# Kernel tuning notes

Measured on AMD Instinct MI355X. Metric: run time of the kernel, lower is better.

The kernel has to match this reference:

```python
import jax, jax.numpy as jnp
import numpy as np

V, D, F, B, E = 50257, 1024, 2048, 64, 512  # vocab, embed/rnn dim, fc hidden, batch, entities


def setup_inputs() -> dict:
    key = jax.random.key(0)
    ks = jax.random.split(key, 12)
    s = 0.05
    return {
        "entity_hiddens": jax.random.normal(ks[0], (B, E, D), jnp.float32),
        "question": jax.random.randint(ks[1], (B,), 0, V),
        "keys_mask": jax.random.randint(ks[2], (B, E), 0, 2).astype(bool),
        "emb": jax.random.normal(ks[3], (V, D), jnp.float32) * s,
        "W1": jax.random.normal(ks[4], (D, F), jnp.float32) * s,
        "b1": jnp.zeros((F,), jnp.float32),
        "W2": jax.random.normal(ks[5], (F, D), jnp.float32) * s,
        "b2": jnp.zeros((D,), jnp.float32),
        "A": jax.random.normal(ks[6], (D, D), jnp.float32) * s,  # entity_attn_matrix
        "H": jax.random.normal(ks[7], (D, D), jnp.float32) * s,
        "Ws": jax.random.normal(ks[8], (D, V), jnp.float32) * s,
        "bs": jnp.zeros((V,), jnp.float32),
    }


def reference(entity_hiddens, question, keys_mask, emb, W1, b1, W2, b2, A, H, Ws, bs):
    # embed question token and project: [B, D]
    eq0 = emb[question]
    q = jax.nn.relu(eq0 @ W1 + b1) @ W2 + b2
    # attention_entities actual returned math:
    # reduce_sum(expand_dims(q@A,1) * boolean_mask(entities, mask), axis=1)
    # == (q @ A) * sum over all masked entities (a single [D] vector)
    qA = q @ A  # [B, D]
    m = keys_mask.astype(entity_hiddens.dtype)
    ent_sum = jnp.sum(entity_hiddens * m[..., None], axis=(0, 1))  # [D]
    u = qA * ent_sum  # [B, D]
    logits = (q + u @ H) @ Ws + bs  # [B, V]
    return jax.nn.softmax(logits, axis=-1)
```

## Files before the change

kernel.cpp:

```cpp
#include <hip/hip_runtime.h>
#include <stdint.h>

#define V_ 50257
#define D_ 1024
#define F_ 2048
#define B_ 64
#define E_ 512
#define ROWS_ (B_*E_)

typedef __attribute__((ext_vector_type(8))) short bf16x8;
typedef __attribute__((ext_vector_type(4))) float f32x4;

__device__ __forceinline__ unsigned rne1(float a) {
  unsigned u = __float_as_uint(a);
  return (u + 0x7FFFu + ((u >> 16) & 1u)) >> 16;
}

__device__ __forceinline__ float waveMax(float v) {
#pragma unroll
  for (int o = 32; o > 0; o >>= 1) v = fmaxf(v, __shfl_xor(v, o, 64));
  return v;
}
__device__ __forceinline__ float waveSum(float v) {
#pragma unroll
  for (int o = 32; o > 0; o >>= 1) v += __shfl_xor(v, o, 64);
  return v;
}


__device__ __forceinline__ void ent_partial_body(int bid, const float* __restrict__ eh,
                                                 const void* __restrict__ mask,
                                                 float* __restrict__ part) {
  __shared__ int s_mode;
  const int tid = threadIdx.x;
  const uint32_t* mu = (const uint32_t*)mask;
  int f = 0;
  for (int i = tid; i < (ROWS_ / 4); i += 256) {
    uint32_t u = mu[i];
    if (u == 0x3F800000u) f |= 2;
    else if (u & 0xFFFFFF00u) f |= 1;
  }
  if (tid == 0) s_mode = 0;
  __syncthreads();
  if (f) atomicOr(&s_mode, f);
  __syncthreads();
  const int sm = s_mode;
  const int mode = (sm & 1) ? 1 : ((sm & 2) ? 2 : 0);

  float4 acc = make_float4(0.f, 0.f, 0.f, 0.f);
  const float4* eh4 = (const float4*)eh;
  for (int row = bid; row < ROWS_; row += 512) {
    bool on;
    if (mode == 1)      on = ((const unsigned char*)mask)[row] != 0;
    else if (mode == 2) on = ((const float*)mask)[row] != 0.f;
    else                on = ((const int*)mask)[row] != 0;
    if (on) {
      float4 v = eh4[(size_t)row * (D_ / 4) + tid];
      acc.x += v.x; acc.y += v.y; acc.z += v.z; acc.w += v.w;
    }
  }
  ((float4*)part)[(size_t)bid * (D_ / 4) + tid] = acc;
}

__device__ __forceinline__ void ent_reduce_body(int bid, const float* __restrict__ part,
                                                float* __restrict__ entsum) {
  int d = bid * 256 + threadIdx.x;
  float s0 = 0.f, s1 = 0.f, s2 = 0.f, s3 = 0.f;
  for (int i = 0; i < 512; i += 4) {
    s0 += part[(size_t)(i    ) * D_ + d];
    s1 += part[(size_t)(i + 1) * D_ + d];
    s2 += part[(size_t)(i + 2) * D_ + d];
    s3 += part[(size_t)(i + 3) * D_ + d];
  }
  entsum[d] = (s0 + s1) + (s2 + s3);
}

__device__ __forceinline__ void gemm64_body(int bx, int by, const float* __restrict__ X,
                                            const int* __restrict__ gatherIdx,
                                            const float* __restrict__ emb,
                                            const float* __restrict__ W,
                                            int K, int N, int KB, float* __restrict__ part) {
  const int l  = threadIdx.x & 63;
  const int rg = __builtin_amdgcn_readfirstlane((int)(threadIdx.x >> 6));
  const int c  = bx * 64 + l;
  const int k0 = by * KB;
  const int m0 = rg * 16;

  const float* Xp = gatherIdx ? emb : X;
  int rb[16];
#pragma unroll
  for (int r = 0; r < 16; ++r) {
    int m = m0 + r;
    rb[r] = gatherIdx ? gatherIdx[m] * K : m * K;
  }

  float acc[16];
#pragma unroll
  for (int r = 0; r < 16; ++r) acc[r] = 0.f;

  for (int k = k0; k < k0 + KB; k += 8) {
    float wv[8];
#pragma unroll
    for (int j = 0; j < 8; ++j) wv[j] = W[(size_t)(k + j) * N + c];
#pragma unroll
    for (int r = 0; r < 16; ++r) {
      float4 x0 = *(const float4*)&Xp[rb[r] + k];
      float4 x1 = *(const float4*)&Xp[rb[r] + k + 4];
      acc[r] = fmaf(x0.x, wv[0], acc[r]);
      acc[r] = fmaf(x0.y, wv[1], acc[r]);
      acc[r] = fmaf(x0.z, wv[2], acc[r]);
      acc[r] = fmaf(x0.w, wv[3], acc[r]);
      acc[r] = fmaf(x1.x, wv[4], acc[r]);
      acc[r] = fmaf(x1.y, wv[5], acc[r]);
      acc[r] = fmaf(x1.z, wv[6], acc[r]);
      acc[r] = fmaf(x1.w, wv[7], acc[r]);
    }
  }
  size_t base = (size_t)by * ((size_t)64 * N);
#pragma unroll
  for (int r = 0; r < 16; ++r) part[base + (size_t)(m0 + r) * N + c] = acc[r];
}

__device__ __forceinline__ void reduce_ep_body(int bid, const float* __restrict__ part,
                                               int nsplit, int MN, int N,
                                               const float* __restrict__ vecB,
                                               const float* __restrict__ addend,
                                               int mode, float* __restrict__ dst,
                                               unsigned short* __restrict__ dhi,
                                               unsigned short* __restrict__ dlo) {
  int idx = bid * 256 + threadIdx.x;
  if (idx >= MN) return;
  float s = 0.f;
  for (int i = 0; i < nsplit; ++i) s += part[(size_t)i * MN + idx];
  int c = idx & (N - 1);
  if (mode == 1)      { s += vecB[c]; s = s > 0.f ? s : 0.f; dst[idx] = s; }
  else if (mode == 2) { s += vecB[c]; dst[idx] = s; }
  else if (mode == 3) { s *= vecB[c]; dst[idx] = s; }
  else {
    s += addend[idx];
    unsigned hi = rne1(s);
    float hif = __uint_as_float(hi << 16);
    dhi[idx] = (unsigned short)hi;
    dlo[idx] = (unsigned short)rne1(s - hif);
  }
}

__global__ void k_p1(const float* __restrict__ eh, const void* __restrict__ mask,
                     float* __restrict__ entpart, const int* __restrict__ ques,
                     const float* __restrict__ emb, const float* __restrict__ W1,
                     float* __restrict__ gpart) {
  int bid = blockIdx.x;
  if (bid < 512) ent_partial_body(bid, eh, mask, entpart);
  else {
    int b2 = bid - 512;
    gemm64_body(b2 & 31, b2 >> 5, nullptr, ques, emb, W1, 1024, 2048, 64, gpart);
  }
}

__global__ void k_p2(const float* __restrict__ entpart, float* __restrict__ entsum,
                     const float* __restrict__ gpart, const float* __restrict__ b1,
                     float* __restrict__ hbuf) {
  int bid = blockIdx.x;
  if (bid < 4) ent_reduce_body(bid, entpart, entsum);
  else reduce_ep_body(bid - 4, gpart, 16, 64 * 2048, 2048, b1, nullptr, 1, hbuf, nullptr, nullptr);
}

__global__ void k_gemm64(const float* __restrict__ X, const float* __restrict__ W,
                         int K, int N, int KB, float* __restrict__ part) {
  gemm64_body(blockIdx.x, blockIdx.y, X, nullptr, nullptr, W, K, N, KB, part);
}

__global__ void k_reduce_ep(const float* __restrict__ part, int nsplit, int MN, int N,
                            const float* __restrict__ vecB, const float* __restrict__ addend,
                            int mode, float* __restrict__ dst,
                            unsigned short* __restrict__ dhi, unsigned short* __restrict__ dlo) {
  reduce_ep_body(blockIdx.x, part, nsplit, MN, N, vecB, addend, mode, dst, dhi, dlo);
}

__global__ __launch_bounds__(512, 1) void k_gemm_big(const unsigned short* __restrict__ zhi,
                                                     const unsigned short* __restrict__ zlo,
                                                     const float* __restrict__ Ws,
                                                     float* __restrict__ part2) {
  __shared__ float lds[2][32 * 514];
  const int t   = threadIdx.x;
  const int l   = t & 63;
  const int w   = t >> 6;
  const int col = l & 15;
  const int g   = l >> 4;
  const int c0  = blockIdx.x * 512;
  const int kbase = blockIdx.y * 512;

  int scol[8];
#pragma unroll
  for (int j = 0; j < 8; ++j) {
    int s = c0 + j * 64 + l;
    scol[j] = s < V_ ? s : V_ - 1;
  }

  unsigned aoff[4];
#pragma unroll
  for (int m = 0; m < 4; ++m) aoff[m] = (unsigned)((m * 16 + col) * D_ + g * 8);

  f32x4 acc[4][4];
#pragma unroll
  for (int n = 0; n < 4; ++n)
#pragma unroll
    for (int m = 0; m < 4; ++m) acc[n][m] = (f32x4){0.f, 0.f, 0.f, 0.f};

#pragma unroll
  for (int i = 0; i < 4; ++i) {
    const int r = w * 4 + i;
#pragma unroll
    for (int j = 0; j < 8; ++j) {
      __builtin_amdgcn_global_load_lds(
          (const __attribute__((address_space(1))) void*)(Ws + (size_t)(kbase + r) * V_ + scol[j]),
          (__attribute__((address_space(3))) void*)&lds[0][r * 514 + j * 64],
          4, 0, 0);
    }
  }
  __syncthreads();

  for (int it = 0; it < 16; ++it) {
    const int buf = it & 1;
    const int k0  = kbase + it * 32;

    bf16x8 ah[4], al[4];
#pragma unroll
    for (int m = 0; m < 4; ++m) {
      ah[m] = *(const bf16x8*)(zhi + aoff[m] + k0);
      al[m] = *(const bf16x8*)(zlo + aoff[m] + k0);
    }

    if (it + 1 < 16) {
      const float* wb = Ws + (size_t)(k0 + 32) * V_;
#pragma unroll
      for (int i = 0; i < 4; ++i) {
        const int r = w * 4 + i;
#pragma unroll
        for (int j = 0; j < 8; ++j) {
          __builtin_amdgcn_global_load_lds(
              (const __attribute__((address_space(1))) void*)(wb + (size_t)r * V_ + scol[j]),
              (__attribute__((address_space(3))) void*)&lds[buf ^ 1][r * 514 + j * 64],
              4, 0, 0);
        }
      }
    }

#pragma unroll
    for (int n = 0; n < 4; ++n) {
      float f[8];
#pragma unroll
      for (int j = 0; j < 8; ++j)
        f[j] = lds[buf][(g * 8 + j) * 514 + w * 64 + n * 16 + col];

      union { bf16x8 v; unsigned u[4]; } bh, bl;
#pragma unroll
      for (int j = 0; j < 4; ++j) {
        unsigned h0 = rne1(f[2 * j]);
        unsigned h1 = rne1(f[2 * j + 1]);
        float h0f = __uint_as_float(h0 << 16);
        float h1f = __uint_as_float(h1 << 16);
        bh.u[j] = h0 | (h1 << 16);
        bl.u[j] = rne1(f[2 * j] - h0f) | (rne1(f[2 * j + 1] - h1f) << 16);
      }
#pragma unroll
      for (int m = 0; m < 4; ++m) acc[n][m] = __builtin_amdgcn_mfma_f32_16x16x32_bf16(ah[m], bh.v, acc[n][m], 0, 0, 0);
#pragma unroll
      for (int m = 0; m < 4; ++m) acc[n][m] = __builtin_amdgcn_mfma_f32_16x16x32_bf16(ah[m], bl.v, acc[n][m], 0, 0, 0);
#pragma unroll
      for (int m = 0; m < 4; ++m) acc[n][m] = __builtin_amdgcn_mfma_f32_16x16x32_bf16(al[m], bh.v, acc[n][m], 0, 0, 0);
    }

    __syncthreads();
  }

  float* pout = part2 + (size_t)blockIdx.y * ((size_t)64 * V_);
#pragma unroll
  for (int n = 0; n < 4; ++n) {
    const int c = c0 + w * 64 + n * 16 + col;
    if (c < V_) {
#pragma unroll
      for (int m = 0; m < 4; ++m)
#pragma unroll
        for (int i = 0; i < 4; ++i)
          pout[(size_t)(m * 16 + g * 4 + i) * V_ + c] = acc[n][m][i];
    }
  }
}

#define SM_CHUNK 12565

__global__ void k_redbias(const float* __restrict__ part2, const float* __restrict__ bs,
                          float* __restrict__ logits) {
  const int r = blockIdx.x >> 2, q = blockIdx.x & 3;
  const int beg = q * SM_CHUNK;
  const int end = (beg + SM_CHUNK < V_) ? beg + SM_CHUNK : V_;
  const float* p0 = part2 + (size_t)r * V_;
  const float* p1 = part2 + (size_t)64 * V_ + (size_t)r * V_;
  float* orow = logits + (size_t)r * V_;
  for (int i = beg + threadIdx.x; i < end; i += 256) orow[i] = p0[i] + p1[i] + bs[i];
}


__global__ void k_softmax1(const float* __restrict__ logits, float2* __restrict__ stats) {
  __shared__ float smx[4], ssum[4];
  const int r = blockIdx.x >> 2, q = blockIdx.x & 3;
  const int beg = q * SM_CHUNK;
  const int end = (beg + SM_CHUNK < V_) ? beg + SM_CHUNK : V_;
  const float* row = logits + (size_t)r * V_;

  float mx = -3.4e38f;
  for (int i = beg + threadIdx.x; i < end; i += 256) mx = fmaxf(mx, row[i]);
  mx = waveMax(mx);
  if ((threadIdx.x & 63) == 0) smx[threadIdx.x >> 6] = mx;
  __syncthreads();
  mx = fmaxf(fmaxf(smx[0], smx[1]), fmaxf(smx[2], smx[3]));

  float s = 0.f;
  for (int i = beg + threadIdx.x; i < end; i += 256) s += __expf(row[i] - mx);
  s = waveSum(s);
  if ((threadIdx.x & 63) == 0) ssum[threadIdx.x >> 6] = s;
  __syncthreads();
  s = (ssum[0] + ssum[1]) + (ssum[2] + ssum[3]);

  if (threadIdx.x == 0) stats[blockIdx.x] = make_float2(mx, s);
}

__global__ void k_softmax2(const float* __restrict__ logits, const float2* __restrict__ stats,
                           float* __restrict__ out) {
  const int r = blockIdx.x >> 2, q = blockIdx.x & 3;
  float2 s0 = stats[r * 4 + 0], s1 = stats[r * 4 + 1];
  float2 s2 = stats[r * 4 + 2], s3 = stats[r * 4 + 3];
  float M = fmaxf(fmaxf(s0.x, s1.x), fmaxf(s2.x, s3.x));
  float S = s0.y * __expf(s0.x - M) + s1.y * __expf(s1.x - M)
          + s2.y * __expf(s2.x - M) + s3.y * __expf(s3.x - M);
  float inv = 1.f / S;
  const int beg = q * SM_CHUNK;
  const int end = (beg + SM_CHUNK < V_) ? beg + SM_CHUNK : V_;
  const float* row = logits + (size_t)r * V_;
  float* orow = out + (size_t)r * V_;
  for (int i = beg + threadIdx.x; i < end; i += 256) orow[i] = __expf(row[i] - M) * inv;
}

extern "C" void kernel_launch(void* const* d_in, const int* in_sizes, int n_in,
                              void* d_out, int out_size, void* d_ws, size_t ws_size,
                              hipStream_t stream) {
  const float* eh   = (const float*)d_in[0];
  const int*   ques = (const int*)d_in[1];
  const void*  mask = d_in[2];
  const float* emb  = (const float*)d_in[3];
  const float* W1   = (const float*)d_in[4];
  const float* b1   = (const float*)d_in[5];
  const float* W2   = (const float*)d_in[6];
  const float* b2   = (const float*)d_in[7];
  const float* A    = (const float*)d_in[8];
  const float* H    = (const float*)d_in[9];
  const float* Ws   = (const float*)d_in[10];
  const float* bs   = (const float*)d_in[11];
  float* out = (float*)d_out;
  char* ws = (char*)d_ws;

  float*          logits  = (float*)(ws + 0);
  float*          gpart   = (float*)(ws + 0);
  float*          entpart = (float*)(ws + 12866048);
  float*          entsum  = (float*)(ws + 14963200);
  float*          hbuf    = (float*)(ws + 14967296);
  float*          qbuf    = (float*)(ws + 15491584);
  float*          ubuf    = (float*)(ws + 15753728);
  unsigned short* zhi16   = (unsigned short*)(ws + 16015872);
  unsigned short* zlo16   = (unsigned short*)(ws + 16146944);
  float2*         stats   = (float2*)(ws + 16278016);
  float*          part2   = (float*)(ws + 20971520);

  k_p1<<<1024, 256, 0, stream>>>(eh, mask, entpart, ques, emb, W1, gpart);
  k_p2<<<516, 256, 0, stream>>>(entpart, entsum, gpart, b1, hbuf);

  k_gemm64<<<dim3(16, 32), 256, 0, stream>>>(hbuf, W2, 2048, 1024, 64, gpart);
  k_reduce_ep<<<256, 256, 0, stream>>>(gpart, 32, 64 * 1024, 1024, b2, nullptr, 2, qbuf, nullptr, nullptr);

  k_gemm64<<<dim3(16, 16), 256, 0, stream>>>(qbuf, A, 1024, 1024, 64, gpart);
  k_reduce_ep<<<256, 256, 0, stream>>>(gpart, 16, 64 * 1024, 1024, entsum, nullptr, 3, ubuf, nullptr, nullptr);

  k_gemm64<<<dim3(16, 16), 256, 0, stream>>>(ubuf, H, 1024, 1024, 64, gpart);
  k_reduce_ep<<<256, 256, 0, stream>>>(gpart, 16, 64 * 1024, 1024, nullptr, qbuf, 4, nullptr, zhi16, zlo16);

  k_gemm_big<<<dim3(99, 2), 512, 0, stream>>>(zhi16, zlo16, Ws, part2);
  k_redbias<<<256, 256, 0, stream>>>(part2, bs, logits);

  k_softmax1<<<256, 256, 0, stream>>>(logits, stats);
  k_softmax2<<<256, 256, 0, stream>>>(logits, stats, out);

  (void)in_sizes; (void)n_in; (void)out_size; (void)ws_size;
}
```

Before: 273.9 us.

## Stage Ws tiles via vectorized register loads instead of per-element LDS DMA

The big vocab GEMM used 4-byte global_load_lds per element to fill the Ws tile. It now loads 16-byte vectors into registers, issuing them before the MFMA loop and writing them to the other LDS buffer afterwards, with sched barriers keeping that order. The last column block is shifted to end at V so no clamped loads are needed, and the LDS row pitch changes to 516 to keep vector stores aligned. This raises register pressure and makes the last block overlap columns already computed by its neighbour; those duplicate outputs get written twice.

```diff
diff --git a/kernel.cpp b/kernel.cpp
--- a/kernel.cpp
+++ b/kernel.cpp
@@ -10,6 +10,7 @@
 
 typedef __attribute__((ext_vector_type(8))) short bf16x8;
 typedef __attribute__((ext_vector_type(4))) float f32x4;
+typedef __attribute__((ext_vector_type(4), aligned(4))) float f32x4a;
 
 __device__ __forceinline__ unsigned rne1(float a) {
   unsigned u = __float_as_uint(a);
@@ -181,21 +182,17 @@
                                                      const unsigned short* __restrict__ zlo,
                                                      const float* __restrict__ Ws,
                                                      float* __restrict__ part2) {
-  __shared__ float lds[2][32 * 514];
+  __shared__ float lds[2][32 * 516];
   const int t   = threadIdx.x;
   const int l   = t & 63;
   const int w   = t >> 6;
   const int col = l & 15;
   const int g   = l >> 4;
-  const int c0  = blockIdx.x * 512;
+  const int c0  = (blockIdx.x < 98) ? blockIdx.x * 512 : (V_ - 512);
   const int kbase = blockIdx.y * 512;
 
-  int scol[8];
-#pragma unroll
-  for (int j = 0; j < 8; ++j) {
-    int s = c0 + j * 64 + l;
-    scol[j] = s < V_ ? s : V_ - 1;
-  }
+  const int rr0 = t >> 7;
+  const int ccf = (t & 127) * 4;
 
   unsigned aoff[4];
 #pragma unroll
@@ -207,22 +204,24 @@
 #pragma unroll
     for (int m = 0; m < 4; ++m) acc[n][m] = (f32x4){0.f, 0.f, 0.f, 0.f};
 
-#pragma unroll
-  for (int i = 0; i < 4; ++i) {
-    const int r = w * 4 + i;
-#pragma unroll
-    for (int j = 0; j < 8; ++j) {
-      __builtin_amdgcn_global_load_lds(
-          (const __attribute__((address_space(1))) void*)(Ws + (size_t)(kbase + r) * V_ + scol[j]),
-          (__attribute__((address_space(3))) void*)&lds[0][r * 514 + j * 64],
-          4, 0, 0);
-    }
-  }
-  __syncthreads();
-
-  for (int it = 0; it < 16; ++it) {
-    const int buf = it & 1;
-    const int k0  = kbase + it * 32;
+  {
+    f32x4a gg[8];
+#pragma unroll
+    for (int r8 = 0; r8 < 8; ++r8) {
+      const int r = r8 * 4 + rr0;
+      gg[r8] = *(const f32x4a*)(Ws + (size_t)(kbase + r) * V_ + c0 + ccf);
+    }
+#pragma unroll
+    for (int r8 = 0; r8 < 8; ++r8) {
+      const int r = r8 * 4 + rr0;
+      *(f32x4*)&lds[0][r * 516 + ccf] = (f32x4)gg[r8];
+    }
+  }
+  __syncthreads();
+
+  for (int tt = 0; tt < 16; ++tt) {
+    const int buf = tt & 1;
+    const int k0  = kbase + tt * 32;
 
     bf16x8 ah[4], al[4];
 #pragma unroll
@@ -231,27 +230,21 @@
       al[m] = *(const bf16x8*)(zlo + aoff[m] + k0);
     }
 
-    if (it + 1 < 16) {
-      const float* wb = Ws + (size_t)(k0 + 32) * V_;
-#pragma unroll
-      for (int i = 0; i < 4; ++i) {
-        const int r = w * 4 + i;
-#pragma unroll
-        for (int j = 0; j < 8; ++j) {
-          __builtin_amdgcn_global_load_lds(
-              (const __attribute__((address_space(1))) void*)(wb + (size_t)r * V_ + scol[j]),
-              (__attribute__((address_space(3))) void*)&lds[buf ^ 1][r * 514 + j * 64],
-              4, 0, 0);
-        }
-      }
-    }
+    f32x4a gg[8];
+    if (tt + 1 < 16) {
+      const float* wb = Ws + (size_t)(k0 + 32) * V_ + c0 + ccf;
+#pragma unroll
+      for (int r8 = 0; r8 < 8; ++r8)
+        gg[r8] = *(const f32x4a*)(wb + (size_t)(r8 * 4 + rr0) * V_);
+    }
+    __builtin_amdgcn_sched_barrier(0);
 
 #pragma unroll
     for (int n = 0; n < 4; ++n) {
       float f[8];
 #pragma unroll
       for (int j = 0; j < 8; ++j)
-        f[j] = lds[buf][(g * 8 + j) * 514 + w * 64 + n * 16 + col];
+        f[j] = lds[buf][(g * 8 + j) * 516 + w * 64 + n * 16 + col];
 
       union { bf16x8 v; unsigned u[4]; } bh, bl;
 #pragma unroll
@@ -270,7 +263,15 @@
 #pragma unroll
       for (int m = 0; m < 4; ++m) acc[n][m] = __builtin_amdgcn_mfma_f32_16x16x32_bf16(al[m], bh.v, acc[n][m], 0, 0, 0);
     }
-
+    __builtin_amdgcn_sched_barrier(0);
+
+    if (tt + 1 < 16) {
+#pragma unroll
+      for (int r8 = 0; r8 < 8; ++r8) {
+        const int r = r8 * 4 + rr0;
+        *(f32x4*)&lds[buf ^ 1][r * 516 + ccf] = (f32x4)gg[r8];
+      }
+    }
     __syncthreads();
   }
 
```

New measurement: 268.7 us. About the same (-1.9%).
